# Optimization experiments

Measured on AMD Instinct MI355X. Metric: run time of the kernel, lower is better.

Reference implementation:

```python
import jax, jax.numpy as jnp
import numpy as np

NUM_GRAPHS = 512


def setup_inputs() -> dict:
    key = jax.random.key(0)
    ks = jax.random.split(key, 8)
    N, H, Ep, En = 100000, 160, 500000, 500000
    x = jax.random.normal(ks[0], (N, H), dtype=jnp.float32)
    pos_edge_index = jax.random.randint(ks[1], (2, Ep), 0, N, dtype=jnp.int32)
    neg_edge_index = jax.random.randint(ks[2], (2, En), 0, N, dtype=jnp.int32)
    batch = jnp.sort(jax.random.randint(ks[3], (N,), 0, NUM_GRAPHS, dtype=jnp.int32))
    # decoder params: Linear(H,H) then Linear(H,1), torch default uniform init
    s = 1.0 / np.sqrt(H)
    W1 = jax.random.uniform(ks[4], (H, H), jnp.float32, -s, s)
    b1 = jax.random.uniform(ks[5], (H,), jnp.float32, -s, s)
    W2 = jax.random.uniform(ks[6], (1, H), jnp.float32, -s, s)
    b2 = jax.random.uniform(ks[7], (1,), jnp.float32, -s, s)
    return {"x": x, "pos_edge_index": pos_edge_index, "neg_edge_index": neg_edge_index,
            "batch": batch, "W1": W1, "b1": b1, "W2": W2, "b2": b2}


def _bce(p, t):
    # torch BCELoss clamps log terms at -100
    return -(t * jnp.maximum(jnp.log(p), -100.0)
             + (1.0 - t) * jnp.maximum(jnp.log1p(-p), -100.0))


def reference(x, pos_edge_index, neg_edge_index, batch, W1, b1, W2, b2):
    Ep = pos_edge_index.shape[1]
    i_idx = jnp.concatenate([pos_edge_index[0], neg_edge_index[0]])
    j_idx = jnp.concatenate([pos_edge_index[1], neg_edge_index[1]])
    # Sequential: ReLU -> Linear(H,H) -> ReLU -> Linear(H,1)
    h = jax.nn.relu(x[i_idx] * x[j_idx])                 # [E, H]
    h = jax.nn.relu(h @ W1.T + b1)                        # [E, H]
    logits = h @ W2.T + b2                                # [E, 1]
    pred = (logits > 0.5).astype(x.dtype)                 # straight-through threshold
    pos_pred, neg_pred = pred[:Ep], pred[Ep:]
    pos_loss = _bce(pos_pred, jnp.ones_like(pos_pred))    # [Ep, 1]
    neg_loss = _bce(neg_pred, jnp.zeros_like(neg_pred))   # [En, 1]
    loss_pos = jax.ops.segment_sum(pos_loss, batch[pos_edge_index[0]], num_segments=NUM_GRAPHS)
    loss_neg = jax.ops.segment_sum(neg_loss, batch[neg_edge_index[0]], num_segments=NUM_GRAPHS)
    return (loss_pos + loss_neg).mean()
```

## Files before the change

### kernel.cpp

```cpp
#include <hip/hip_runtime.h>

typedef float f32x4 __attribute__((ext_vector_type(4)));
typedef float f32x2 __attribute__((ext_vector_type(2)));
typedef short s16x8 __attribute__((ext_vector_type(8)));
typedef unsigned int u32;
typedef unsigned int u32x2 __attribute__((ext_vector_type(2)));

#define HDIM 160
#define NT 10
#define KS 5
#define CHF 10
#define STAGE_I 5
#define BUFB (32 * HDIM)

__device__ __forceinline__ unsigned short f2bf(float f) {
    union { float f; unsigned u; } v; v.f = f;
    unsigned u = v.u;
    return (unsigned short)((u + 0x7FFFu + ((u >> 16) & 1u)) >> 16);
}

__global__ void prep_x_fp8(const float* __restrict__ x,
                           u32* __restrict__ xf8,
                           int* __restrict__ counter, int n8) {
    int idx = blockIdx.x * blockDim.x + threadIdx.x;
    if (idx == 0) *counter = 0;
    if (idx < n8) {
        f32x4 a = ((const f32x4*)x)[idx * 2];
        f32x4 b = ((const f32x4*)x)[idx * 2 + 1];
        u32 lo = __builtin_amdgcn_cvt_pk_fp8_f32(a.x, a.y, 0u, false);
        lo = __builtin_amdgcn_cvt_pk_fp8_f32(a.z, a.w, lo, true);
        u32 hi = __builtin_amdgcn_cvt_pk_fp8_f32(b.x, b.y, 0u, false);
        hi = __builtin_amdgcn_cvt_pk_fp8_f32(b.z, b.w, hi, true);
        u32x2 o; o.x = lo; o.y = hi;
        ((u32x2*)xf8)[idx] = o;
    }
}

__global__ void zero_kernel(int* __restrict__ counter) {
    if (threadIdx.x == 0) *counter = 0;
}

__global__ __launch_bounds__(64, 2) void gae_main_fp8(
    const u32* __restrict__ xf8,
    const int* __restrict__ pos,
    const int* __restrict__ neg,
    const float* __restrict__ W1,
    const float* __restrict__ b1,
    const float* __restrict__ W2,
    const float* __restrict__ b2,
    int* __restrict__ counter,
    int Ep, int En) {
    __shared__ char rowbuf[3][BUFB];
    __shared__ int idxlds[3][64];

    const int E = Ep + En;
    const int lane = threadIdx.x;
    const int c = lane & 15;
    const int q = lane >> 4;
    const int D = gridDim.x;
    const int numIter = (E + 15) >> 4;

    u32 bfr_lo[KS][NT], bfr_hi[KS][NT];
#pragma unroll
    for (int s = 0; s < KS; s++) {
#pragma unroll
        for (int n = 0; n < NT; n++) {
            const float* wp = W1 + (size_t)(n * 16 + c) * HDIM + 32 * s + 8 * q;
            f32x4 w0 = *(const f32x4*)wp;
            f32x4 w1v = *(const f32x4*)(wp + 4);
            u32 lo = __builtin_amdgcn_cvt_pk_fp8_f32(w0.x, w0.y, 0u, false);
            lo = __builtin_amdgcn_cvt_pk_fp8_f32(w0.z, w0.w, lo, true);
            u32 hi = __builtin_amdgcn_cvt_pk_fp8_f32(w1v.x, w1v.y, 0u, false);
            hi = __builtin_amdgcn_cvt_pk_fp8_f32(w1v.z, w1v.w, hi, true);
            bfr_lo[s][n] = lo; bfr_hi[s][n] = hi;
        }
    }

    float b1r[NT], w2r[NT];
#pragma unroll
    for (int n = 0; n < NT; n++) {
        b1r[n] = b1[n * 16 + c];
        w2r[n] = W2[n * 16 + c];
    }
    const float b2v = b2[0];

    int rArr4[STAGE_I];
    int dOff[STAGE_I];
#pragma unroll
    for (int tt = 0; tt < STAGE_I; tt++) {
        int f = tt * 64 + lane;
        int r = (f * 6554) >> 16;
        int cp = f - 10 * r;
        int r10 = r - 10 * ((r * 6554) >> 16);
        int d = cp - r10;
        d += (d < 0) ? CHF : 0;
        rArr4[tt] = r * 4;
        dOff[tt] = d * 16;
    }

#define STAGE_IDX(T, SLOT)                                               \
    {                                                                    \
        int e = ((T) << 4) + (lane & 15);                                \
        e = (e < E) ? e : (E - 1);                                       \
        const int* bi = (e < Ep) ? (pos + e) : (neg + (e - Ep));         \
        const int* bj = (e < Ep) ? (pos + Ep + e) : (neg + En + (e - Ep)); \
        const int* srcI = ((lane >> 4) & 1) ? bj : bi;                   \
        __builtin_amdgcn_global_load_lds(                                \
            (const __attribute__((address_space(1))) void*)srcI,         \
            (__attribute__((address_space(3))) void*)(&idxlds[SLOT][0]), \
            4, 0, 0);                                                    \
    }

#define STAGE_ROWS(RSLOT, ISLOT)                                         \
    {                                                                    \
        const char* ib = (const char*)&idxlds[ISLOT][0];                 \
        char* rb = rowbuf[RSLOT];                                        \
        _Pragma("unroll")                                                \
        for (int tt = 0; tt < STAGE_I; tt++) {                           \
            int rowIdx = *(const int*)(ib + rArr4[tt]);                  \
            const char* src =                                            \
                (const char*)(xf8) + (size_t)rowIdx * HDIM + dOff[tt];   \
            __builtin_amdgcn_global_load_lds(                            \
                (const __attribute__((address_space(1))) void*)src,      \
                (__attribute__((address_space(3))) void*)(rb + tt * 1024),\
                16, 0, 0);                                               \
        }                                                                \
    }

    int cnt = 0;
    int t = blockIdx.x;

    STAGE_IDX(t, 0);
    STAGE_IDX(t + D, 1);
    __builtin_amdgcn_s_waitcnt(0x0F70);
    STAGE_ROWS(0, 0);
    STAGE_IDX(t + 2 * D, 0);
    STAGE_ROWS(1, 1);
    STAGE_IDX(t + 3 * D, 1);

    int p = 0;
    for (; t < numIter; t += D) {
        const int e0 = t << 4;
        int p2 = p + 2; p2 -= (p2 >= 3) ? 3 : 0;

        __builtin_amdgcn_sched_barrier(0);
        __builtin_amdgcn_s_waitcnt(0x0F76);
        __builtin_amdgcn_sched_barrier(0);

        STAGE_ROWS(p2, p);
        STAGE_IDX(t + 4 * D, p2);
        __builtin_amdgcn_sched_barrier(0);

        const char* buf = rowbuf[p];
        f32x4 acc[NT];
#pragma unroll
        for (int n = 0; n < NT; n++) acc[n] = (f32x4)(0.0f);

#pragma unroll
        for (int s = 0; s < KS; s++) {
            int d = 2 * s + (q >> 1);
            int off8 = 8 * (q & 1);
            int pi = d + c;
            pi -= (pi >= CHF) ? CHF : 0;
            pi -= (pi >= CHF) ? CHF : 0;
            int pj = d + 6 + c;
            pj -= (pj >= CHF) ? CHF : 0;
            pj -= (pj >= CHF) ? CHF : 0;
            pj -= (pj >= CHF) ? CHF : 0;
            u32x2 iw = *(const u32x2*)(buf + c * HDIM + pi * 16 + off8);
            u32x2 jw = *(const u32x2*)(buf + (16 + c) * HDIM + pj * 16 + off8);
            f32x2 i01 = __builtin_amdgcn_cvt_pk_f32_fp8(iw.x, false);
            f32x2 i23 = __builtin_amdgcn_cvt_pk_f32_fp8(iw.x, true);
            f32x2 i45 = __builtin_amdgcn_cvt_pk_f32_fp8(iw.y, false);
            f32x2 i67 = __builtin_amdgcn_cvt_pk_f32_fp8(iw.y, true);
            f32x2 j01 = __builtin_amdgcn_cvt_pk_f32_fp8(jw.x, false);
            f32x2 j23 = __builtin_amdgcn_cvt_pk_f32_fp8(jw.x, true);
            f32x2 j45 = __builtin_amdgcn_cvt_pk_f32_fp8(jw.y, false);
            f32x2 j67 = __builtin_amdgcn_cvt_pk_f32_fp8(jw.y, true);
            float p0 = fmaxf(i01.x * j01.x, 0.0f);
            float p1 = fmaxf(i01.y * j01.y, 0.0f);
            float p2f = fmaxf(i23.x * j23.x, 0.0f);
            float p3 = fmaxf(i23.y * j23.y, 0.0f);
            float p4 = fmaxf(i45.x * j45.x, 0.0f);
            float p5 = fmaxf(i45.y * j45.y, 0.0f);
            float p6 = fmaxf(i67.x * j67.x, 0.0f);
            float p7 = fmaxf(i67.y * j67.y, 0.0f);
            u32 alo = __builtin_amdgcn_cvt_pk_fp8_f32(p0, p1, 0u, false);
            alo = __builtin_amdgcn_cvt_pk_fp8_f32(p2f, p3, alo, true);
            u32 ahi = __builtin_amdgcn_cvt_pk_fp8_f32(p4, p5, 0u, false);
            ahi = __builtin_amdgcn_cvt_pk_fp8_f32(p6, p7, ahi, true);
            long afr = (long)(((unsigned long long)ahi << 32) |
                              (unsigned long long)alo);
#pragma unroll
            for (int n = 0; n < NT; n++) {
                long bf8 = (long)(((unsigned long long)bfr_hi[s][n] << 32) |
                                  (unsigned long long)bfr_lo[s][n]);
                acc[n] = __builtin_amdgcn_mfma_f32_16x16x32_fp8_fp8(
                    afr, bf8, acc[n], 0, 0, 0);
            }
        }

        float sArr[4] = {0.0f, 0.0f, 0.0f, 0.0f};
#pragma unroll
        for (int n = 0; n < NT; n++) {
#pragma unroll
            for (int r = 0; r < 4; r++) {
                sArr[r] += fmaxf(acc[n][r] + b1r[n], 0.0f) * w2r[n];
            }
        }
#pragma unroll
        for (int r = 0; r < 4; r++) {
            float sv = sArr[r];
            sv += __shfl_xor(sv, 1);
            sv += __shfl_xor(sv, 2);
            sv += __shfl_xor(sv, 4);
            sv += __shfl_xor(sv, 8);
            if (c == 0) {
                int ge = e0 + q * 4 + r;
                if (ge < E) {
                    float logit = sv + b2v;
                    bool miss = (ge < Ep) ? (logit <= 0.5f) : (logit > 0.5f);
                    cnt += miss ? 1 : 0;
                }
            }
        }

        p = p + 1; p -= (p >= 3) ? 3 : 0;
    }
    __builtin_amdgcn_s_waitcnt(0x0F70);

    cnt += __shfl_xor(cnt, 1);
    cnt += __shfl_xor(cnt, 2);
    cnt += __shfl_xor(cnt, 4);
    cnt += __shfl_xor(cnt, 8);
    cnt += __shfl_xor(cnt, 16);
    cnt += __shfl_xor(cnt, 32);
    if (lane == 0) atomicAdd(counter, cnt);
#undef STAGE_IDX
#undef STAGE_ROWS
}

#define STAGE_F 20
#define BUFNF (32 * HDIM)
__global__ __launch_bounds__(64, 1) void gae_main_f32(
    const float* __restrict__ x,
    const int* __restrict__ pos,
    const int* __restrict__ neg,
    const float* __restrict__ W1,
    const float* __restrict__ b1,
    const float* __restrict__ W2,
    const float* __restrict__ b2,
    int* __restrict__ counter,
    int Ep, int En) {
    __shared__ float rowbuf[2][BUFNF];
    const int E = Ep + En;
    const int lane = threadIdx.x;
    const int c = lane & 15;
    const int q = lane >> 4;
    const int D = gridDim.x;
    const int numIter = (E + 15) >> 4;

    s16x8 bfr[KS][NT];
#pragma unroll
    for (int s = 0; s < KS; s++) {
#pragma unroll
        for (int n = 0; n < NT; n++) {
            const float* wp = W1 + (size_t)(n * 16 + c) * HDIM + 32 * s + 8 * q;
            f32x4 w0 = *(const f32x4*)wp;
            f32x4 w1v = *(const f32x4*)(wp + 4);
#pragma unroll
            for (int e = 0; e < 4; e++) {
                bfr[s][n][e]     = (short)f2bf(w0[e]);
                bfr[s][n][e + 4] = (short)f2bf(w1v[e]);
            }
        }
    }
    float b1r[NT], w2r[NT];
#pragma unroll
    for (int n = 0; n < NT; n++) { b1r[n] = b1[n*16+c]; w2r[n] = W2[n*16+c]; }
    const float b2v = b2[0];

#define LOAD_IDXF(T, I, J) { int e = ((T) << 4) + c; e = (e < E) ? e : (E-1); \
    const int* bi = (e < Ep) ? (pos + e) : (neg + (e - Ep)); \
    const int* bj = (e < Ep) ? (pos + Ep + e) : (neg + En + (e - Ep)); \
    (I) = *bi; (J) = *bj; }
#define STAGEF(IA, JA, BUF) { _Pragma("unroll") \
    for (int tt = 0; tt < STAGE_F; tt++) { \
        int f = tt * 64 + lane; \
        int r = (f * 1639) >> 16; \
        int cp = f - 40 * r; \
        int cs = cp - r; cs = (cs < 0) ? cs + 40 : cs; \
        int ri = __shfl((IA), r); \
        int rj = __shfl((JA), r); \
        int rowIdx = (r < 16) ? ri : rj; \
        const float* src = x + (size_t)rowIdx * HDIM + cs * 4; \
        __builtin_amdgcn_global_load_lds( \
            (const __attribute__((address_space(1))) void*)src, \
            (__attribute__((address_space(3))) void*)((BUF) + tt * 256), \
            16, 0, 0); } }

    int cnt = 0;
    int t = blockIdx.x;
    int iC, jC, iN, jN;
    if (t < numIter) {
        LOAD_IDXF(t, iC, jC);
        STAGEF(iC, jC, rowbuf[0]);
        LOAD_IDXF(t + D, iN, jN);
        __builtin_amdgcn_s_waitcnt(0x0F70);
    }
    int p = 0;
    for (; t < numIter; t += D) {
        const int e0 = t << 4;
        STAGEF(iN, jN, rowbuf[p ^ 1]);
        int i2, j2;
        LOAD_IDXF(t + 2 * D, i2, j2);
        __builtin_amdgcn_sched_barrier(0);
        const float* buf = rowbuf[p];
        f32x4 acc[NT];
#pragma unroll
        for (int n = 0; n < NT; n++) acc[n] = (f32x4)(0.0f);
#pragma unroll
        for (int s = 0; s < KS; s++) {
            const int c8 = 8 * s + 2 * q;
            int p0 = c8 + c;       p0 -= (p0 >= 40) ? 40 : 0;
            int p1 = c8 + 1 + c;   p1 -= (p1 >= 40) ? 40 : 0;
            int pj0 = c8 + 16 + c; pj0 -= (pj0 >= 40) ? 40 : 0;
            int pj1 = c8 + 17 + c; pj1 -= (pj1 >= 40) ? 40 : 0;
            f32x4 u0 = *(const f32x4*)(buf + c * HDIM + p0 * 4);
            f32x4 u1 = *(const f32x4*)(buf + c * HDIM + p1 * 4);
            f32x4 v0 = *(const f32x4*)(buf + (16 + c) * HDIM + pj0 * 4);
            f32x4 v1 = *(const f32x4*)(buf + (16 + c) * HDIM + pj1 * 4);
            s16x8 af;
#pragma unroll
            for (int e = 0; e < 4; e++) {
                af[e]     = (short)f2bf(fmaxf(u0[e] * v0[e], 0.0f));
                af[e + 4] = (short)f2bf(fmaxf(u1[e] * v1[e], 0.0f));
            }
#pragma unroll
            for (int n = 0; n < NT; n++)
                acc[n] = __builtin_amdgcn_mfma_f32_16x16x32_bf16(af, bfr[s][n], acc[n], 0, 0, 0);
        }
        float sArr[4] = {0.0f, 0.0f, 0.0f, 0.0f};
#pragma unroll
        for (int n = 0; n < NT; n++)
#pragma unroll
            for (int r = 0; r < 4; r++)
                sArr[r] += fmaxf(acc[n][r] + b1r[n], 0.0f) * w2r[n];
#pragma unroll
        for (int r = 0; r < 4; r++) {
            float sv = sArr[r];
            sv += __shfl_xor(sv, 1);
            sv += __shfl_xor(sv, 2);
            sv += __shfl_xor(sv, 4);
            sv += __shfl_xor(sv, 8);
            if (c == 0) {
                int ge = e0 + q * 4 + r;
                if (ge < E) {
                    float logit = sv + b2v;
                    bool miss = (ge < Ep) ? (logit <= 0.5f) : (logit > 0.5f);
                    cnt += miss ? 1 : 0;
                }
            }
        }
        iN = i2; jN = j2;
        __builtin_amdgcn_s_waitcnt(0x0F70);
        __builtin_amdgcn_sched_barrier(0);
        p ^= 1;
    }
    cnt += __shfl_xor(cnt, 1);
    cnt += __shfl_xor(cnt, 2);
    cnt += __shfl_xor(cnt, 4);
    cnt += __shfl_xor(cnt, 8);
    cnt += __shfl_xor(cnt, 16);
    cnt += __shfl_xor(cnt, 32);
    if (lane == 0) atomicAdd(counter, cnt);
#undef LOAD_IDXF
#undef STAGEF
}

__global__ void finalize_kernel(const int* __restrict__ counter,
                                float* __restrict__ out) {
    if (blockIdx.x == 0 && threadIdx.x == 0) {
        out[0] = 100.0f * (float)(*counter) / 512.0f;
    }
}

extern "C" void kernel_launch(void* const* d_in, const int* in_sizes, int n_in,
                              void* d_out, int out_size, void* d_ws, size_t ws_size,
                              hipStream_t stream) {
    const float* x = (const float*)d_in[0];
    const int* pos = (const int*)d_in[1];
    const int* neg = (const int*)d_in[2];
    const float* W1 = (const float*)d_in[4];
    const float* b1 = (const float*)d_in[5];
    const float* W2 = (const float*)d_in[6];
    const float* b2 = (const float*)d_in[7];

    const int Ep = in_sizes[1] / 2;
    const int En = in_sizes[2] / 2;
    const int xn = in_sizes[0];

    int* counter = (int*)d_ws;
    u32* xf8 = (u32*)((char*)d_ws + 256);
    const size_t wsNeeded = 256 + (size_t)xn;

    if (ws_size >= wsNeeded) {
        const int n8 = xn / 8;
        prep_x_fp8<<<(n8 + 255) / 256, 256, 0, stream>>>(x, xf8, counter, n8);
        gae_main_fp8<<<2048, 64, 0, stream>>>(xf8, pos, neg, W1, b1, W2, b2,
                                              counter, Ep, En);
    } else {
        zero_kernel<<<1, 64, 0, stream>>>(counter);
        gae_main_f32<<<1024, 64, 0, stream>>>(x, pos, neg, W1, b1, W2, b2,
                                              counter, Ep, En);
    }
    finalize_kernel<<<1, 64, 0, stream>>>(counter, (float*)d_out);
}
```

Measured before the change: 219.6 us.

## Double-buffer row staging, fuse finalize via last-block atomic, vectorize elementwise math

Row staging in the fp8 path drops from a three-deep to a two-deep LDS ring, which cuts shared memory per block so the grid can grow from 2048 to 3072 blocks. The separate finalize kernel is replaced by a last-block-done atomic counter that writes the output from inside the main kernel, saving one launch. The product/ReLU and bias/ReLU/W2 reductions are rewritten as packed two- and four-wide vector operations, and the prep kernel block size changes. The shallower prefetch hides less gather latency, and the extra fence and atomic add a little serialization at the end of each block.

After: 380.4 us. 1.73x slower.

```diff
diff --git a/kernel.cpp b/kernel.cpp
--- a/kernel.cpp
+++ b/kernel.cpp
@@ -23,7 +23,7 @@
                            u32* __restrict__ xf8,
                            int* __restrict__ counter, int n8) {
     int idx = blockIdx.x * blockDim.x + threadIdx.x;
-    if (idx == 0) *counter = 0;
+    if (idx == 0) { counter[0] = 0; counter[1] = 0; }
     if (idx < n8) {
         f32x4 a = ((const f32x4*)x)[idx * 2];
         f32x4 b = ((const f32x4*)x)[idx * 2 + 1];
@@ -37,7 +37,7 @@
 }
 
 __global__ void zero_kernel(int* __restrict__ counter) {
-    if (threadIdx.x == 0) *counter = 0;
+    if (threadIdx.x == 0) { counter[0] = 0; counter[1] = 0; }
 }
 
 __global__ __launch_bounds__(64, 2) void gae_main_fp8(
@@ -49,9 +49,10 @@
     const float* __restrict__ W2,
     const float* __restrict__ b2,
     int* __restrict__ counter,
+    float* __restrict__ out,
     int Ep, int En) {
-    __shared__ char rowbuf[3][BUFB];
-    __shared__ int idxlds[3][64];
+    __shared__ char rowbuf[2][BUFB];
+    __shared__ int idxlds[2][64];
 
     const int E = Ep + En;
     const int lane = threadIdx.x;
@@ -130,25 +131,23 @@
     int cnt = 0;
     int t = blockIdx.x;
 
-    STAGE_IDX(t, 0);
-    STAGE_IDX(t + D, 1);
-    __builtin_amdgcn_s_waitcnt(0x0F70);
-    STAGE_ROWS(0, 0);
-    STAGE_IDX(t + 2 * D, 0);
-    STAGE_ROWS(1, 1);
-    STAGE_IDX(t + 3 * D, 1);
+    if (t < numIter) {
+        STAGE_IDX(t, 0);
+        __builtin_amdgcn_s_waitcnt(0x0F70);
+        STAGE_ROWS(0, 0);
+        STAGE_IDX(t + D, 1);
+    }
 
     int p = 0;
     for (; t < numIter; t += D) {
         const int e0 = t << 4;
-        int p2 = p + 2; p2 -= (p2 >= 3) ? 3 : 0;
 
         __builtin_amdgcn_sched_barrier(0);
-        __builtin_amdgcn_s_waitcnt(0x0F76);
+        __builtin_amdgcn_s_waitcnt(0x0F70);
         __builtin_amdgcn_sched_barrier(0);
 
-        STAGE_ROWS(p2, p);
-        STAGE_IDX(t + 4 * D, p2);
+        STAGE_ROWS(p ^ 1, p ^ 1);
+        STAGE_IDX(t + 2 * D, p);
         __builtin_amdgcn_sched_barrier(0);
 
         const char* buf = rowbuf[p];
@@ -169,26 +168,23 @@
             pj -= (pj >= CHF) ? CHF : 0;
             u32x2 iw = *(const u32x2*)(buf + c * HDIM + pi * 16 + off8);
             u32x2 jw = *(const u32x2*)(buf + (16 + c) * HDIM + pj * 16 + off8);
-            f32x2 i01 = __builtin_amdgcn_cvt_pk_f32_fp8(iw.x, false);
-            f32x2 i23 = __builtin_amdgcn_cvt_pk_f32_fp8(iw.x, true);
-            f32x2 i45 = __builtin_amdgcn_cvt_pk_f32_fp8(iw.y, false);
-            f32x2 i67 = __builtin_amdgcn_cvt_pk_f32_fp8(iw.y, true);
-            f32x2 j01 = __builtin_amdgcn_cvt_pk_f32_fp8(jw.x, false);
-            f32x2 j23 = __builtin_amdgcn_cvt_pk_f32_fp8(jw.x, true);
-            f32x2 j45 = __builtin_amdgcn_cvt_pk_f32_fp8(jw.y, false);
-            f32x2 j67 = __builtin_amdgcn_cvt_pk_f32_fp8(jw.y, true);
-            float p0 = fmaxf(i01.x * j01.x, 0.0f);
-            float p1 = fmaxf(i01.y * j01.y, 0.0f);
-            float p2f = fmaxf(i23.x * j23.x, 0.0f);
-            float p3 = fmaxf(i23.y * j23.y, 0.0f);
-            float p4 = fmaxf(i45.x * j45.x, 0.0f);
-            float p5 = fmaxf(i45.y * j45.y, 0.0f);
-            float p6 = fmaxf(i67.x * j67.x, 0.0f);
-            float p7 = fmaxf(i67.y * j67.y, 0.0f);
-            u32 alo = __builtin_amdgcn_cvt_pk_fp8_f32(p0, p1, 0u, false);
-            alo = __builtin_amdgcn_cvt_pk_fp8_f32(p2f, p3, alo, true);
-            u32 ahi = __builtin_amdgcn_cvt_pk_fp8_f32(p4, p5, 0u, false);
-            ahi = __builtin_amdgcn_cvt_pk_fp8_f32(p6, p7, ahi, true);
+            f32x2 pa = __builtin_amdgcn_cvt_pk_f32_fp8(iw.x, false) *
+                       __builtin_amdgcn_cvt_pk_f32_fp8(jw.x, false);
+            f32x2 pb = __builtin_amdgcn_cvt_pk_f32_fp8(iw.x, true) *
+                       __builtin_amdgcn_cvt_pk_f32_fp8(jw.x, true);
+            f32x2 pc = __builtin_amdgcn_cvt_pk_f32_fp8(iw.y, false) *
+                       __builtin_amdgcn_cvt_pk_f32_fp8(jw.y, false);
+            f32x2 pd = __builtin_amdgcn_cvt_pk_f32_fp8(iw.y, true) *
+                       __builtin_amdgcn_cvt_pk_f32_fp8(jw.y, true);
+            const f32x2 z2 = (f32x2)(0.0f);
+            pa = __builtin_elementwise_max(pa, z2);
+            pb = __builtin_elementwise_max(pb, z2);
+            pc = __builtin_elementwise_max(pc, z2);
+            pd = __builtin_elementwise_max(pd, z2);
+            u32 alo = __builtin_amdgcn_cvt_pk_fp8_f32(pa.x, pa.y, 0u, false);
+            alo = __builtin_amdgcn_cvt_pk_fp8_f32(pb.x, pb.y, alo, true);
+            u32 ahi = __builtin_amdgcn_cvt_pk_fp8_f32(pc.x, pc.y, 0u, false);
+            ahi = __builtin_amdgcn_cvt_pk_fp8_f32(pd.x, pd.y, ahi, true);
             long afr = (long)(((unsigned long long)ahi << 32) |
                               (unsigned long long)alo);
 #pragma unroll
@@ -200,17 +196,17 @@
             }
         }
 
-        float sArr[4] = {0.0f, 0.0f, 0.0f, 0.0f};
+        f32x4 sVec = (f32x4)(0.0f);
+        const f32x4 z4 = (f32x4)(0.0f);
 #pragma unroll
         for (int n = 0; n < NT; n++) {
-#pragma unroll
-            for (int r = 0; r < 4; r++) {
-                sArr[r] += fmaxf(acc[n][r] + b1r[n], 0.0f) * w2r[n];
-            }
+            f32x4 v = acc[n] + (f32x4)(b1r[n]);
+            v = __builtin_elementwise_max(v, z4);
+            sVec += v * (f32x4)(w2r[n]);
         }
 #pragma unroll
         for (int r = 0; r < 4; r++) {
-            float sv = sArr[r];
+            float sv = sVec[r];
             sv += __shfl_xor(sv, 1);
             sv += __shfl_xor(sv, 2);
             sv += __shfl_xor(sv, 4);
@@ -225,7 +221,7 @@
             }
         }
 
-        p = p + 1; p -= (p >= 3) ? 3 : 0;
+        p ^= 1;
     }
     __builtin_amdgcn_s_waitcnt(0x0F70);
 
@@ -235,7 +231,15 @@
     cnt += __shfl_xor(cnt, 8);
     cnt += __shfl_xor(cnt, 16);
     cnt += __shfl_xor(cnt, 32);
-    if (lane == 0) atomicAdd(counter, cnt);
+    if (lane == 0) {
+        atomicAdd(counter, cnt);
+        __threadfence();
+        int done = atomicAdd(counter + 1, 1) + 1;
+        if (done == (int)gridDim.x) {
+            int total = atomicAdd(counter, 0);
+            out[0] = 100.0f * (float)total / 512.0f;
+        }
+    }
 #undef STAGE_IDX
 #undef STAGE_ROWS
 }
@@ -406,13 +410,13 @@
 
     if (ws_size >= wsNeeded) {
         const int n8 = xn / 8;
-        prep_x_fp8<<<(n8 + 255) / 256, 256, 0, stream>>>(x, xf8, counter, n8);
-        gae_main_fp8<<<2048, 64, 0, stream>>>(xf8, pos, neg, W1, b1, W2, b2,
-                                              counter, Ep, En);
+        prep_x_fp8<<<(n8 + 511) / 512, 512, 0, stream>>>(x, xf8, counter, n8);
+        gae_main_fp8<<<3072, 64, 0, stream>>>(xf8, pos, neg, W1, b1, W2, b2,
+                                              counter, (float*)d_out, Ep, En);
     } else {
         zero_kernel<<<1, 64, 0, stream>>>(counter);
         gae_main_f32<<<1024, 64, 0, stream>>>(x, pos, neg, W1, b1, W2, b2,
                                               counter, Ep, En);
-    }
-    finalize_kernel<<<1, 64, 0, stream>>>(counter, (float*)d_out);
-}
+        finalize_kernel<<<1, 64, 0, stream>>>(counter, (float*)d_out);
+    }
+}
```
